# Kernel tuning notes

Hardware: AMD Instinct MI355X
Metric: run time of the kernel (lower is better)

The kernel has to match this reference:

```python
import jax, jax.numpy as jnp
import numpy as np

B, S, D, H = 4, 2048, 1024, 16
DH = D // H
MAX_SEQ = 2048
OUT = 1024


def setup_inputs() -> dict:
    key = jax.random.key(0)
    ks = jax.random.split(key, 10)
    inp = {
        "x": jax.random.normal(ks[0], (B, S, D), dtype=jnp.float32),
        "src_key_padding_mask": jnp.ones((B, S), dtype=jnp.float32),  # 1 = valid token
        "pos_emb": jax.random.normal(ks[1], (1, MAX_SEQ, D), dtype=jnp.float32),
        "ln_gamma": jnp.ones((D,), dtype=jnp.float32),
        "ln_beta": jnp.zeros((D,), dtype=jnp.float32),
        "in_proj_weight": jax.random.normal(ks[2], (3 * D, D), dtype=jnp.float32) * (1.0 / np.sqrt(D)),
        "in_proj_bias": jnp.zeros((3 * D,), dtype=jnp.float32),
        "out_proj_weight": jax.random.normal(ks[3], (D, D), dtype=jnp.float32) * (1.0 / np.sqrt(D)),
        "out_proj_bias": jnp.zeros((D,), dtype=jnp.float32),
        "to_out_weight": jax.random.normal(ks[4], (OUT, D), dtype=jnp.float32) * (1.0 / np.sqrt(D)),
        "to_out_bias": jnp.zeros((OUT,), dtype=jnp.float32),
    }
    return inp


def _layernorm(x, gamma, beta, eps=1e-5):
    mu = jnp.mean(x, axis=-1, keepdims=True)
    var = jnp.mean(jnp.square(x - mu), axis=-1, keepdims=True)
    return (x - mu) * jax.lax.rsqrt(var + eps) * gamma + beta


def reference(x, src_key_padding_mask, pos_emb, ln_gamma, ln_beta,
              in_proj_weight, in_proj_bias, out_proj_weight, out_proj_bias,
              to_out_weight, to_out_bias):
    seq = x.shape[1]
    xn = _layernorm(x, ln_gamma, ln_beta)
    xp = xn + pos_emb[:, :seq, :]  # [B,S,D]

    # PyTorch quirk: 1.0 - mask.long() is a FLOAT tensor -> treated as ADDITIVE mask.
    add_mask = (1.0 - src_key_padding_mask)[:, None, None, :]  # [B,1,1,S]

    qkv = xp @ in_proj_weight.T + in_proj_bias  # [B,S,3D]
    q, k, v = jnp.split(qkv, 3, axis=-1)
    # [B,H,S,DH]
    q = q.reshape(B, seq, H, DH).transpose(0, 2, 1, 3)
    k = k.reshape(B, seq, H, DH).transpose(0, 2, 1, 3)
    v = v.reshape(B, seq, H, DH).transpose(0, 2, 1, 3)

    scores = jnp.einsum("bhqd,bhkd->bhqk", q, k) / jnp.sqrt(jnp.float32(DH))
    scores = scores + add_mask
    attn = jax.nn.softmax(scores, axis=-1)
    o = jnp.einsum("bhqk,bhkd->bhqd", attn, v)  # [B,H,S,DH]
    o = o.transpose(0, 2, 1, 3).reshape(B, seq, D)
    attn_out = o @ out_proj_weight.T + out_proj_bias

    return (xp + attn_out) @ to_out_weight.T + to_out_bias
```

## Files before the change

kernel.cpp:

```cpp
#include <hip/hip_runtime.h>
#include <stdint.h>
#include <stddef.h>

typedef unsigned short u16;
typedef __bf16 bf16x8 __attribute__((ext_vector_type(8)));
typedef float floatx4 __attribute__((ext_vector_type(4)));

#define B_  4
#define S_  2048
#define D_  1024
#define H_  16
#define DH_ 64

__device__ __forceinline__ float b2f(u16 u) {
  union { unsigned u; float f; } c; c.u = ((unsigned)u) << 16; return c.f;
}
__device__ __forceinline__ u16 f2b(float f) {
  union { float f; unsigned u; } c; c.f = f;
  unsigned u = c.u;
  u += 0x7fffu + ((u >> 16) & 1u);
  return (u16)(u >> 16);
}

__device__ __forceinline__ void gld_lds16(const u16* g, u16* l) {
  __builtin_amdgcn_global_load_lds(
      (const __attribute__((address_space(1))) unsigned int*)g,
      (__attribute__((address_space(3))) unsigned int*)l, 16, 0, 0);
}

__device__ __forceinline__ unsigned cvtpk(float lo, float hi) {
  unsigned r;
  asm("v_cvt_pk_bf16_f32 %0, %1, %2" : "=v"(r) : "v"(lo), "v"(hi));
  return r;
}

#define PL32(a, b) asm("v_permlane32_swap_b32 %0, %1" : "+v"(a), "+v"(b))
#define PL16(a, b) asm("v_permlane16_swap_b32 %0, %1" : "+v"(a), "+v"(b))

union B8 { unsigned u[4]; bf16x8 v; };

__global__ __launch_bounds__(256) void cvt_f32_bf16(
    const float* __restrict__ src, u16* __restrict__ dst, int n)
{
  int i = (blockIdx.x * 256 + threadIdx.x) * 4;
  if (i >= n) return;
  float4 v = *(const float4*)(src + i);
  u16 o[4] __attribute__((aligned(8)));
  o[0] = f2b(v.x); o[1] = f2b(v.y); o[2] = f2b(v.z); o[3] = f2b(v.w);
  *(uint2*)(dst + i) = *(uint2*)o;
}

__global__ __launch_bounds__(256) void ln_pos_kernel(
    const float* __restrict__ x, const float* __restrict__ pos,
    const float* __restrict__ gamma, const float* __restrict__ beta,
    u16* __restrict__ xp)
{
  const int row = blockIdx.x;
  const int s = row & (S_ - 1);
  const int t = threadIdx.x;
  const int lane = t & 63, w = t >> 6;

  float4 xv = *(const float4*)(x + (size_t)row * D_ + t * 4);
  float f[4] = {xv.x, xv.y, xv.z, xv.w};
  float sum = f[0] + f[1] + f[2] + f[3];
  float sq  = f[0]*f[0] + f[1]*f[1] + f[2]*f[2] + f[3]*f[3];
#pragma unroll
  for (int m = 1; m < 64; m <<= 1) {
    sum += __shfl_xor(sum, m);
    sq  += __shfl_xor(sq, m);
  }
  __shared__ float red[8];
  if (lane == 0) { red[w] = sum; red[4 + w] = sq; }
  __syncthreads();
  sum = red[0] + red[1] + red[2] + red[3];
  sq  = red[4] + red[5] + red[6] + red[7];
  const float mu = sum * (1.f / D_);
  const float rstd = rsqrtf(fmaxf(sq * (1.f / D_) - mu * mu, 0.f) + 1e-5f);

  float4 gv = *(const float4*)(gamma + t * 4);
  float4 bv = *(const float4*)(beta + t * 4);
  float4 pv = *(const float4*)(pos + (size_t)s * D_ + t * 4);
  float g[4] = {gv.x, gv.y, gv.z, gv.w};
  float bb[4] = {bv.x, bv.y, bv.z, bv.w};
  float pp[4] = {pv.x, pv.y, pv.z, pv.w};
  u16 ov[4] __attribute__((aligned(8)));
#pragma unroll
  for (int i = 0; i < 4; ++i)
    ov[i] = f2b((f[i] - mu) * rstd * g[i] + bb[i] + pp[i]);
  *(uint2*)(xp + (size_t)row * D_ + t * 4) = *(uint2*)ov;
}

template<int HAS_BIAS, int HAS_RES, int OUT_F32>
__global__ __launch_bounds__(256) void gemm_bt(
    const u16* A, const u16* __restrict__ Bm,
    const float* __restrict__ bias, const u16* res,
    void* Cv, int M, int N, int K, int lda, int ldc)
{
  __shared__ u16 As[128 * 32];
  __shared__ u16 Bs[128 * 32];
  const int tid = threadIdx.x;
  const int lane = tid & 63, w = tid >> 6;
  const int quad = lane >> 4, l4 = lane & 15;
  const int wm = (w >> 1) * 64, wn = (w & 1) * 64;
  const int m0 = blockIdx.y * 128, n0 = blockIdx.x * 128;

  const u16* Ag = A + (size_t)m0 * lda;
  const u16* Bg = Bm + (size_t)n0 * K;

  const int s0 = tid, s1 = tid + 256;
  const int r0 = s0 >> 2, c0 = ((s0 & 3) - (r0 >> 1)) & 3;
  const int r1 = s1 >> 2, c1 = ((s1 & 3) - (r1 >> 1)) & 3;
  const int pA = (quad + (l4 >> 1)) & 3;

  floatx4 acc[4][4] = {};

  for (int k0 = 0; k0 < K; k0 += 32) {
    __syncthreads();
    gld_lds16(Ag + (size_t)r0 * lda + k0 + c0 * 8, &As[s0 * 8]);
    gld_lds16(Ag + (size_t)r1 * lda + k0 + c1 * 8, &As[s1 * 8]);
    gld_lds16(Bg + (size_t)r0 * K + k0 + c0 * 8, &Bs[s0 * 8]);
    gld_lds16(Bg + (size_t)r1 * K + k0 + c1 * 8, &Bs[s1 * 8]);
    __syncthreads();
    bf16x8 af[4], bfr[4];
#pragma unroll
    for (int i = 0; i < 4; ++i)
      af[i] = *(const bf16x8*)&As[(wm + i * 16 + l4) * 32 + pA * 8];
#pragma unroll
    for (int j = 0; j < 4; ++j)
      bfr[j] = *(const bf16x8*)&Bs[(wn + j * 16 + l4) * 32 + pA * 8];
#pragma unroll
    for (int i = 0; i < 4; ++i)
#pragma unroll
      for (int j = 0; j < 4; ++j)
        acc[i][j] = __builtin_amdgcn_mfma_f32_16x16x32_bf16(af[i], bfr[j], acc[i][j], 0, 0, 0);
  }

#pragma unroll
  for (int i = 0; i < 4; ++i) {
#pragma unroll
    for (int j = 0; j < 4; ++j) {
      const int col = n0 + wn + j * 16 + l4;
      float bvv = 0.f;
      if (HAS_BIAS) bvv = bias[col];
#pragma unroll
      for (int r = 0; r < 4; ++r) {
        const int row = m0 + wm + i * 16 + quad * 4 + r;
        float v = acc[i][j][r] + bvv;
        if (HAS_RES) v += b2f(res[(size_t)row * ldc + col]);
        v = fminf(fmaxf(v, -60000.f), 60000.f);
        if (OUT_F32) ((float*)Cv)[(size_t)row * ldc + col] = v;
        else         ((u16*)Cv)[(size_t)row * ldc + col] = f2b(v);
      }
    }
  }
}

__global__ __launch_bounds__(256, 4) void attn_kernel(
    u16* qkv, const float* __restrict__ mask)
{
  __shared__ u16 Ks[2][64 * 64];
  __shared__ u16 Vt[2][64 * 72];

  const int tid = threadIdx.x;
  const int lane = tid & 63, w = tid >> 6;
  const int quad = lane >> 4, l4 = lane & 15;
  const int qb = blockIdx.x;
  const int bh = blockIdx.y;
  const int b = bh >> 4, h = bh & 15;
  const int q0 = qb * 64;

  const size_t rstr = 3 * D_;
  u16* qbase = qkv + (size_t)b * S_ * rstr + h * DH_;

  bf16x8 qfrag[2];
  {
    const u16* qp = qbase + (size_t)(q0 + w * 16 + l4) * rstr + quad * 8;
    qfrag[0] = *(const bf16x8*)(qp);
    qfrag[1] = *(const bf16x8*)(qp + 32);
  }

  const u16* kbase0 = qkv + (size_t)b * S_ * rstr + D_ + h * DH_;
  const u16* vbase0 = kbase0 + D_;
  const int vs = tid & 63, vd0 = (tid >> 6) * 16;

  floatx4 acc_o[4] = {};
  float l_run = 0.f;
  u16 vreg[16] __attribute__((aligned(16)));

  {
    const u16* kb = kbase0;
#pragma unroll
    for (int t = 0; t < 2; ++t) {
      int sidx = tid + t * 256;
      int rr = sidx >> 3, ch = ((sidx & 7) - rr) & 7;
      gld_lds16(kb + (size_t)rr * rstr + ch * 8, &Ks[0][sidx * 8]);
    }
    const u16* vp = vbase0 + (size_t)vs * rstr + vd0;
    *(uint4*)(vreg)     = *(const uint4*)(vp);
    *(uint4*)(vreg + 8) = *(const uint4*)(vp + 8);
  }
  __syncthreads();
#pragma unroll
  for (int d = 0; d < 16; ++d) Vt[0][(vd0 + d) * 72 + vs] = vreg[d];
  __syncthreads();

  int cur = 0;
  for (int j = 0; j < 32; ++j) {
    if (j < 31) {
      const u16* vp = vbase0 + ((size_t)(j + 1) * 64 + vs) * rstr + vd0;
      *(uint4*)(vreg)     = *(const uint4*)(vp);
      *(uint4*)(vreg + 8) = *(const uint4*)(vp + 8);
      const u16* kb = kbase0 + (size_t)(j + 1) * 64 * rstr;
#pragma unroll
      for (int t = 0; t < 2; ++t) {
        int sidx = tid + t * 256;
        int rr = sidx >> 3, ch = ((sidx & 7) - rr) & 7;
        gld_lds16(kb + (size_t)rr * rstr + ch * 8, &Ks[cur ^ 1][sidx * 8]);
      }
    }

    floatx4 accs[4] = {};
#pragma unroll
    for (int kc = 0; kc < 2; ++kc)
#pragma unroll
      for (int tj = 0; tj < 4; ++tj) {
        const int rk = tj * 16 + l4;
        bf16x8 kf = *(const bf16x8*)&Ks[cur][rk * 64 + (((kc * 4 + quad) + rk) & 7) * 8];
        accs[tj] = __builtin_amdgcn_mfma_f32_16x16x32_bf16(kf, qfrag[kc], accs[tj], 0, 0, 0);
      }

    const float* mrow = mask + (size_t)b * S_ + j * 64 + quad * 4;
    float rsum = 0.f;
    unsigned pk[4][2];
#pragma unroll
    for (int tj = 0; tj < 4; ++tj) {
      float4 mv = *(const float4*)(mrow + tj * 16);
      float p0 = __expf(fminf(fmaf(accs[tj][0], 0.125f, 1.0f - mv.x), 30.f));
      float p1 = __expf(fminf(fmaf(accs[tj][1], 0.125f, 1.0f - mv.y), 30.f));
      float p2 = __expf(fminf(fmaf(accs[tj][2], 0.125f, 1.0f - mv.z), 30.f));
      float p3 = __expf(fminf(fmaf(accs[tj][3], 0.125f, 1.0f - mv.w), 30.f));
      rsum += (p0 + p1) + (p2 + p3);
      pk[tj][0] = cvtpk(p0, p1);
      pk[tj][1] = cvtpk(p2, p3);
    }
    rsum += __shfl_xor(rsum, 16);
    rsum += __shfl_xor(rsum, 32);
    l_run += rsum;

#pragma unroll
    for (int kc = 0; kc < 2; ++kc) {
      unsigned x0 = pk[2 * kc][0], x1 = pk[2 * kc + 1][0];
      unsigned y0 = pk[2 * kc][1], y1 = pk[2 * kc + 1][1];
      PL32(x0, x1); PL32(y0, y1);
      PL16(x0, x1); PL16(y0, y1);
      B8 pa; pa.u[0] = x0; pa.u[1] = y0; pa.u[2] = x1; pa.u[3] = y1;
      __builtin_amdgcn_s_setprio(1);
#pragma unroll
      for (int tn = 0; tn < 4; ++tn) {
        bf16x8 bfr = *(const bf16x8*)&Vt[cur][(tn * 16 + l4) * 72 + kc * 32 + quad * 8];
        acc_o[tn] = __builtin_amdgcn_mfma_f32_16x16x32_bf16(pa.v, bfr, acc_o[tn], 0, 0, 0);
      }
      __builtin_amdgcn_s_setprio(0);
    }

    if (j < 31) {
#pragma unroll
      for (int d = 0; d < 16; ++d) Vt[cur ^ 1][(vd0 + d) * 72 + vs] = vreg[d];
    }

    __syncthreads();
    cur ^= 1;
  }

  float inv[4];
#pragma unroll
  for (int r = 0; r < 4; ++r) inv[r] = 1.0f / __shfl(l_run, quad * 4 + r);
#pragma unroll
  for (int tn = 0; tn < 4; ++tn) {
#pragma unroll
    for (int r = 0; r < 4; ++r) {
      const int row = q0 + w * 16 + quad * 4 + r;
      const int col = h * DH_ + tn * 16 + l4;
      qkv[((size_t)b * S_ + row) * rstr + col] = f2b(acc_o[tn][r] * inv[r]);
    }
  }
}

extern "C" void kernel_launch(void* const* d_in, const int* in_sizes, int n_in,
                              void* d_out, int out_size, void* d_ws, size_t ws_size,
                              hipStream_t stream) {
  const float* x    = (const float*)d_in[0];
  const float* mask = (const float*)d_in[1];
  const float* pos  = (const float*)d_in[2];
  const float* gam  = (const float*)d_in[3];
  const float* bet  = (const float*)d_in[4];
  const float* wqkv = (const float*)d_in[5];
  const float* bqkv = (const float*)d_in[6];
  const float* wo   = (const float*)d_in[7];
  const float* bo   = (const float*)d_in[8];
  const float* wt   = (const float*)d_in[9];
  const float* bt   = (const float*)d_in[10];
  float* out = (float*)d_out;

  char* ws = (char*)d_ws;
  u16* qkvb = (u16*)(ws);
  u16* xp   = (u16*)(ws + (size_t)50331648);

  u16* wqkv_b = (u16*)d_out;
  u16* wo_b   = (u16*)((char*)d_out + (size_t)6291456);
  u16* wt_b   = qkvb;

  const int nqkv = 3 * D_ * D_;
  const int nd   = D_ * D_;

  cvt_f32_bf16<<<nqkv / 1024, 256, 0, stream>>>(wqkv, wqkv_b, nqkv);
  cvt_f32_bf16<<<nd   / 1024, 256, 0, stream>>>(wo,   wo_b,   nd);
  ln_pos_kernel<<<B_ * S_, 256, 0, stream>>>(x, pos, gam, bet, xp);
  gemm_bt<1, 0, 0><<<dim3(3 * D_ / 128, B_ * S_ / 128), 256, 0, stream>>>(
      xp, wqkv_b, bqkv, nullptr, qkvb, B_ * S_, 3 * D_, D_, D_, 3 * D_);
  attn_kernel<<<dim3(S_ / 64, B_ * H_), 256, 0, stream>>>(qkvb, mask);
  gemm_bt<1, 1, 0><<<dim3(D_ / 128, B_ * S_ / 128), 256, 0, stream>>>(
      qkvb, wo_b, bo, xp, xp, B_ * S_, D_, D_, 3 * D_, D_);
  cvt_f32_bf16<<<nd / 1024, 256, 0, stream>>>(wt, wt_b, nd);
  gemm_bt<1, 0, 1><<<dim3(D_ / 128, B_ * S_ / 128), 256, 0, stream>>>(
      xp, wt_b, bt, nullptr, out, B_ * S_, D_, D_, D_, D_);
}
```

Measured before the change: 424.4 us.

## Process 128 query rows per attention block to reuse K/V tiles

```diff
diff --git a/kernel.cpp b/kernel.cpp
--- a/kernel.cpp
+++ b/kernel.cpp
@@ -155,7 +155,7 @@
   }
 }
 
-__global__ __launch_bounds__(256, 4) void attn_kernel(
+__global__ __launch_bounds__(256, 3) void attn_kernel(
     u16* qkv, const float* __restrict__ mask)
 {
   __shared__ u16 Ks[2][64 * 64];
@@ -167,33 +167,33 @@
   const int qb = blockIdx.x;
   const int bh = blockIdx.y;
   const int b = bh >> 4, h = bh & 15;
-  const int q0 = qb * 64;
+  const int q0 = qb * 128;
 
   const size_t rstr = 3 * D_;
   u16* qbase = qkv + (size_t)b * S_ * rstr + h * DH_;
 
-  bf16x8 qfrag[2];
-  {
-    const u16* qp = qbase + (size_t)(q0 + w * 16 + l4) * rstr + quad * 8;
-    qfrag[0] = *(const bf16x8*)(qp);
-    qfrag[1] = *(const bf16x8*)(qp + 32);
+  bf16x8 qfrag[2][2];
+#pragma unroll
+  for (int qi = 0; qi < 2; ++qi) {
+    const u16* qp = qbase + (size_t)(q0 + w * 32 + qi * 16 + l4) * rstr + quad * 8;
+    qfrag[qi][0] = *(const bf16x8*)(qp);
+    qfrag[qi][1] = *(const bf16x8*)(qp + 32);
   }
 
   const u16* kbase0 = qkv + (size_t)b * S_ * rstr + D_ + h * DH_;
   const u16* vbase0 = kbase0 + D_;
   const int vs = tid & 63, vd0 = (tid >> 6) * 16;
 
-  floatx4 acc_o[4] = {};
-  float l_run = 0.f;
+  floatx4 acc_o[2][4] = {};
+  float l_run[2] = {0.f, 0.f};
   u16 vreg[16] __attribute__((aligned(16)));
 
   {
-    const u16* kb = kbase0;
 #pragma unroll
     for (int t = 0; t < 2; ++t) {
       int sidx = tid + t * 256;
       int rr = sidx >> 3, ch = ((sidx & 7) - rr) & 7;
-      gld_lds16(kb + (size_t)rr * rstr + ch * 8, &Ks[0][sidx * 8]);
+      gld_lds16(kbase0 + (size_t)rr * rstr + ch * 8, &Ks[0][sidx * 8]);
     }
     const u16* vp = vbase0 + (size_t)vs * rstr + vd0;
     *(uint4*)(vreg)     = *(const uint4*)(vp);
@@ -219,48 +219,59 @@
       }
     }
 
-    floatx4 accs[4] = {};
+    floatx4 accs[2][4] = {};
 #pragma unroll
     for (int kc = 0; kc < 2; ++kc)
 #pragma unroll
       for (int tj = 0; tj < 4; ++tj) {
         const int rk = tj * 16 + l4;
         bf16x8 kf = *(const bf16x8*)&Ks[cur][rk * 64 + (((kc * 4 + quad) + rk) & 7) * 8];
-        accs[tj] = __builtin_amdgcn_mfma_f32_16x16x32_bf16(kf, qfrag[kc], accs[tj], 0, 0, 0);
+        accs[0][tj] = __builtin_amdgcn_mfma_f32_16x16x32_bf16(kf, qfrag[0][kc], accs[0][tj], 0, 0, 0);
+        accs[1][tj] = __builtin_amdgcn_mfma_f32_16x16x32_bf16(kf, qfrag[1][kc], accs[1][tj], 0, 0, 0);
       }
 
     const float* mrow = mask + (size_t)b * S_ + j * 64 + quad * 4;
-    float rsum = 0.f;
-    unsigned pk[4][2];
-#pragma unroll
-    for (int tj = 0; tj < 4; ++tj) {
-      float4 mv = *(const float4*)(mrow + tj * 16);
-      float p0 = __expf(fminf(fmaf(accs[tj][0], 0.125f, 1.0f - mv.x), 30.f));
-      float p1 = __expf(fminf(fmaf(accs[tj][1], 0.125f, 1.0f - mv.y), 30.f));
-      float p2 = __expf(fminf(fmaf(accs[tj][2], 0.125f, 1.0f - mv.z), 30.f));
-      float p3 = __expf(fminf(fmaf(accs[tj][3], 0.125f, 1.0f - mv.w), 30.f));
-      rsum += (p0 + p1) + (p2 + p3);
-      pk[tj][0] = cvtpk(p0, p1);
-      pk[tj][1] = cvtpk(p2, p3);
-    }
-    rsum += __shfl_xor(rsum, 16);
-    rsum += __shfl_xor(rsum, 32);
-    l_run += rsum;
+    float4 mv[4];
+#pragma unroll
+    for (int tj = 0; tj < 4; ++tj) mv[tj] = *(const float4*)(mrow + tj * 16);
+    unsigned pk[2][4][2];
+#pragma unroll
+    for (int qi = 0; qi < 2; ++qi) {
+      float rsum = 0.f;
+#pragma unroll
+      for (int tj = 0; tj < 4; ++tj) {
+        float p0 = __expf(fminf(fmaf(accs[qi][tj][0], 0.125f, 1.0f - mv[tj].x), 30.f));
+        float p1 = __expf(fminf(fmaf(accs[qi][tj][1], 0.125f, 1.0f - mv[tj].y), 30.f));
+        float p2 = __expf(fminf(fmaf(accs[qi][tj][2], 0.125f, 1.0f - mv[tj].z), 30.f));
+        float p3 = __expf(fminf(fmaf(accs[qi][tj][3], 0.125f, 1.0f - mv[tj].w), 30.f));
+        rsum += (p0 + p1) + (p2 + p3);
+        pk[qi][tj][0] = cvtpk(p0, p1);
+        pk[qi][tj][1] = cvtpk(p2, p3);
+      }
+      rsum += __shfl_xor(rsum, 16);
+      rsum += __shfl_xor(rsum, 32);
+      l_run[qi] += rsum;
+    }
 
 #pragma unroll
     for (int kc = 0; kc < 2; ++kc) {
-      unsigned x0 = pk[2 * kc][0], x1 = pk[2 * kc + 1][0];
-      unsigned y0 = pk[2 * kc][1], y1 = pk[2 * kc + 1][1];
-      PL32(x0, x1); PL32(y0, y1);
-      PL16(x0, x1); PL16(y0, y1);
-      B8 pa; pa.u[0] = x0; pa.u[1] = y0; pa.u[2] = x1; pa.u[3] = y1;
-      __builtin_amdgcn_s_setprio(1);
-#pragma unroll
-      for (int tn = 0; tn < 4; ++tn) {
-        bf16x8 bfr = *(const bf16x8*)&Vt[cur][(tn * 16 + l4) * 72 + kc * 32 + quad * 8];
-        acc_o[tn] = __builtin_amdgcn_mfma_f32_16x16x32_bf16(pa.v, bfr, acc_o[tn], 0, 0, 0);
-      }
-      __builtin_amdgcn_s_setprio(0);
+      bf16x8 bfr[4];
+#pragma unroll
+      for (int tn = 0; tn < 4; ++tn)
+        bfr[tn] = *(const bf16x8*)&Vt[cur][(tn * 16 + l4) * 72 + kc * 32 + quad * 8];
+#pragma unroll
+      for (int qi = 0; qi < 2; ++qi) {
+        unsigned x0 = pk[qi][2 * kc][0], x1 = pk[qi][2 * kc + 1][0];
+        unsigned y0 = pk[qi][2 * kc][1], y1 = pk[qi][2 * kc + 1][1];
+        PL32(x0, x1); PL32(y0, y1);
+        PL16(x0, x1); PL16(y0, y1);
+        B8 pa; pa.u[0] = x0; pa.u[1] = y0; pa.u[2] = x1; pa.u[3] = y1;
+        __builtin_amdgcn_s_setprio(1);
+#pragma unroll
+        for (int tn = 0; tn < 4; ++tn)
+          acc_o[qi][tn] = __builtin_amdgcn_mfma_f32_16x16x32_bf16(pa.v, bfr[tn], acc_o[qi][tn], 0, 0, 0);
+        __builtin_amdgcn_s_setprio(0);
+      }
     }
 
     if (j < 31) {
@@ -272,16 +283,19 @@
     cur ^= 1;
   }
 
-  float inv[4];
-#pragma unroll
-  for (int r = 0; r < 4; ++r) inv[r] = 1.0f / __shfl(l_run, quad * 4 + r);
-#pragma unroll
-  for (int tn = 0; tn < 4; ++tn) {
-#pragma unroll
-    for (int r = 0; r < 4; ++r) {
-      const int row = q0 + w * 16 + quad * 4 + r;
-      const int col = h * DH_ + tn * 16 + l4;
-      qkv[((size_t)b * S_ + row) * rstr + col] = f2b(acc_o[tn][r] * inv[r]);
+#pragma unroll
+  for (int qi = 0; qi < 2; ++qi) {
+    float inv[4];
+#pragma unroll
+    for (int r = 0; r < 4; ++r) inv[r] = 1.0f / __shfl(l_run[qi], quad * 4 + r);
+#pragma unroll
+    for (int tn = 0; tn < 4; ++tn) {
+#pragma unroll
+      for (int r = 0; r < 4; ++r) {
+        const int row = q0 + w * 32 + qi * 16 + quad * 4 + r;
+        const int col = h * DH_ + tn * 16 + l4;
+        qkv[((size_t)b * S_ + row) * rstr + col] = f2b(acc_o[qi][tn][r] * inv[r]);
+      }
     }
   }
 }
@@ -318,7 +332,7 @@
   ln_pos_kernel<<<B_ * S_, 256, 0, stream>>>(x, pos, gam, bet, xp);
   gemm_bt<1, 0, 0><<<dim3(3 * D_ / 128, B_ * S_ / 128), 256, 0, stream>>>(
       xp, wqkv_b, bqkv, nullptr, qkvb, B_ * S_, 3 * D_, D_, D_, 3 * D_);
-  attn_kernel<<<dim3(S_ / 64, B_ * H_), 256, 0, stream>>>(qkvb, mask);
+  attn_kernel<<<dim3(S_ / 128, B_ * H_), 256, 0, stream>>>(qkvb, mask);
   gemm_bt<1, 1, 0><<<dim3(D_ / 128, B_ * S_ / 128), 256, 0, stream>>>(
       qkvb, wo_b, bo, xp, xp, B_ * S_, D_, D_, 3 * D_, D_);
   cvt_f32_bf16<<<nd / 1024, 256, 0, stream>>>(wt, wt_b, nd);
```

New measurement: 409.9 us. 1.04x faster.
